# Optimization experiments

Measured on AMD Instinct MI355X. Metric: run time of the kernel, lower is better.

Reference implementation:

```python
import jax, jax.numpy as jnp
import numpy as np

B, N, D = 8, 2048, 128  # D = d + 2
N_LAYER, N_HEAD = 4, 8
PARAMS_STD = 0.05


def _attention(V, Q, Z):
    # V, Q: [D, D]; Z: [B, N, D]
    n = Z.shape[1]
    Attn = jnp.einsum('bni,ij,bmj->bnm', Z, Q, Z)      # [B, N, N]
    values = jnp.einsum('ij,bnj->bni', V, Z)            # [B, N, D]
    return jnp.einsum('bnm,bmi->bni', Attn, values) / n


def setup_inputs() -> dict:
    key = jax.random.key(0)
    kz, kv, kq = jax.random.split(key, 3)
    Z = jax.random.normal(kz, (B, N, D), dtype=jnp.float32)
    v_matrix = PARAMS_STD * jax.random.normal(kv, (N_LAYER, N_HEAD, 1, D, D), dtype=jnp.float32)
    q_matrix = PARAMS_STD * jax.random.normal(kq, (N_LAYER, N_HEAD, 1, D, D), dtype=jnp.float32)
    return {"Z": Z, "v_matrix": v_matrix, "q_matrix": q_matrix}


def reference(Z, v_matrix, q_matrix):
    n_layer, n_head = v_matrix.shape[0], v_matrix.shape[1]
    for i in range(n_layer):
        Zi = Z
        residues = jnp.zeros_like(Zi)
        for j in range(n_head):  # fixed small head loop keeps peak memory at one [B,N,N] buffer
            Vij = v_matrix[i, j, 0]
            Qij = q_matrix[i, j, 0]
            residues = residues + _attention(Vij, Qij, Zi)
        Z = Zi + residues / n_head
    return Z
```

## Files before the change

kernel.cpp:

```cpp
#include <hip/hip_runtime.h>


constexpr int B  = 8;
constexpr int N  = 2048;
constexpr int D  = 128;
constexpr int NL = 4;
constexpr int NH = 8;
constexpr int SP = 32;
constexpr int RPS = N / SP;
constexpr int PAD = 132;

__global__ __launch_bounds__(1024, 1) void k_gram(const float* __restrict__ Zl,
                                                  float* __restrict__ Gpart) {
  const int s = blockIdx.x, b = blockIdx.y;
  const int t = threadIdx.x;
  __shared__ float zs[RPS][PAD];
  const float* Zb = Zl + ((size_t)b * N + (size_t)s * RPS) * D;
#pragma unroll
  for (int j = 0; j < 2; ++j) {
    int fi = t + j * 1024;
    int row = fi >> 5, c4 = fi & 31;
    *(float4*)&zs[row][c4 * 4] = ((const float4*)Zb)[fi];
  }
  __syncthreads();
  const int ti = t >> 5, tj = t & 31;
  float g[4][4];
#pragma unroll
  for (int i = 0; i < 4; ++i)
#pragma unroll
    for (int j = 0; j < 4; ++j) g[i][j] = 0.0f;
#pragma unroll 4
  for (int k = 0; k < RPS; ++k) {
    float a[4], bb[4];
    *(float4*)&a[0]  = *(const float4*)&zs[k][ti * 4];
    *(float4*)&bb[0] = *(const float4*)&zs[k][tj * 4];
#pragma unroll
    for (int i = 0; i < 4; ++i)
#pragma unroll
      for (int j = 0; j < 4; ++j)
        g[i][j] = fmaf(a[i], bb[j], g[i][j]);
  }
  float* out = Gpart + ((size_t)b * SP + s) * D * D;
#pragma unroll
  for (int i = 0; i < 4; ++i)
    *(float4*)&out[(ti * 4 + i) * D + tj * 4] =
        make_float4(g[i][0], g[i][1], g[i][2], g[i][3]);
}

__global__ __launch_bounds__(1024, 1) void k_gred(const float* __restrict__ Gpart,
                                                  float* __restrict__ G) {
  const int s = blockIdx.x, b = blockIdx.y;
  const int t = threadIdx.x;
  const int wlin = b * SP + s;
  __shared__ float4 cbuf[8][128];
  const int sq = t >> 7;
  const int f  = t & 127;
  int f4 = wlin * 128 + f;
  int b2 = f4 >> 12, rest = f4 & 4095;
  const float4* src = (const float4*)Gpart;
  float4 a = make_float4(0.f, 0.f, 0.f, 0.f);
#pragma unroll
  for (int k = 0; k < 4; ++k) {
    int sp = sq * 4 + k;
    float4 v = src[(size_t)(b2 * SP + sp) * (D * D / 4) + rest];
    a.x += v.x; a.y += v.y; a.z += v.z; a.w += v.w;
  }
  cbuf[sq][f] = a;
  __syncthreads();
  if (t < 128) {
    float4 acc = make_float4(0.f, 0.f, 0.f, 0.f);
#pragma unroll
    for (int g2 = 0; g2 < 8; ++g2) {
      float4 v = cbuf[g2][t];
      acc.x += v.x; acc.y += v.y; acc.z += v.z; acc.w += v.w;
    }
    ((float4*)G)[wlin * 128 + t] = acc;
  }
}

__global__ __launch_bounds__(1024, 1) void k_qgwv(const float* __restrict__ Ql,
                                                  const float* __restrict__ Vl,
                                                  const float* __restrict__ G,
                                                  float* __restrict__ W) {
  const int s = blockIdx.x, b = blockIdx.y;
  const int t = threadIdx.x;
  __shared__ float cbuf[32][D];
  const float* Gb = G + (size_t)b * D * D;
  const int p0 = s * 4;
  {
    const int h  = t >> 7;
    const int pp = (t >> 6) & 1;
    const int c2 = t & 63;
    const int pa = pp * 2, pb = pp * 2 + 1;
    const float* Qa = Ql + ((size_t)h * D + (p0 + pa)) * D;
    const float* Qb = Ql + ((size_t)h * D + (p0 + pb)) * D;
    float ua0 = 0.f, ua1 = 0.f, ub0 = 0.f, ub1 = 0.f;
    for (int q4 = 0; q4 < 32; ++q4) {
      float4 qa = *(const float4*)&Qa[q4 * 4];
      float4 qb = *(const float4*)&Qb[q4 * 4];
      float2 g0 = *(const float2*)&Gb[(size_t)(q4 * 4 + 0) * D + 2 * c2];
      float2 g1 = *(const float2*)&Gb[(size_t)(q4 * 4 + 1) * D + 2 * c2];
      float2 g2 = *(const float2*)&Gb[(size_t)(q4 * 4 + 2) * D + 2 * c2];
      float2 g3 = *(const float2*)&Gb[(size_t)(q4 * 4 + 3) * D + 2 * c2];
      ua0 = fmaf(qa.x, g0.x, ua0); ua1 = fmaf(qa.x, g0.y, ua1);
      ub0 = fmaf(qb.x, g0.x, ub0); ub1 = fmaf(qb.x, g0.y, ub1);
      ua0 = fmaf(qa.y, g1.x, ua0); ua1 = fmaf(qa.y, g1.y, ua1);
      ub0 = fmaf(qb.y, g1.x, ub0); ub1 = fmaf(qb.y, g1.y, ub1);
      ua0 = fmaf(qa.z, g2.x, ua0); ua1 = fmaf(qa.z, g2.y, ua1);
      ub0 = fmaf(qb.z, g2.x, ub0); ub1 = fmaf(qb.z, g2.y, ub1);
      ua0 = fmaf(qa.w, g3.x, ua0); ua1 = fmaf(qa.w, g3.y, ua1);
      ub0 = fmaf(qb.w, g3.x, ub0); ub1 = fmaf(qb.w, g3.y, ub1);
    }
    *(float2*)&cbuf[h * 4 + pa][2 * c2] = make_float2(ua0, ua1);
    *(float2*)&cbuf[h * 4 + pb][2 * c2] = make_float2(ub0, ub1);
  }
  __syncthreads();
  {
    const int w = t >> 6, lane = t & 63;
    const float scale = 1.0f / ((float)N * (float)NH);
    float* Wb = W + (size_t)b * D * D;
    for (int ii = 0; ii < 8; ++ii) {
      const int i = w * 8 + ii;
      float a0 = 0.f, a1 = 0.f, a2 = 0.f, a3 = 0.f;
#pragma unroll
      for (int h = 0; h < NH; ++h) {
        float2 v  = *(const float2*)&Vl[((size_t)h * D + i) * D + 2 * lane];
        float2 u0 = *(const float2*)&cbuf[h * 4 + 0][2 * lane];
        float2 u1 = *(const float2*)&cbuf[h * 4 + 1][2 * lane];
        float2 u2 = *(const float2*)&cbuf[h * 4 + 2][2 * lane];
        float2 u3 = *(const float2*)&cbuf[h * 4 + 3][2 * lane];
        a0 = fmaf(u0.x, v.x, a0); a0 = fmaf(u0.y, v.y, a0);
        a1 = fmaf(u1.x, v.x, a1); a1 = fmaf(u1.y, v.y, a1);
        a2 = fmaf(u2.x, v.x, a2); a2 = fmaf(u2.y, v.y, a2);
        a3 = fmaf(u3.x, v.x, a3); a3 = fmaf(u3.y, v.y, a3);
      }
#pragma unroll
      for (int off = 32; off >= 1; off >>= 1) {
        a0 += __shfl_xor(a0, off, 64);
        a1 += __shfl_xor(a1, off, 64);
        a2 += __shfl_xor(a2, off, 64);
        a3 += __shfl_xor(a3, off, 64);
      }
      if (lane == 0) {
        Wb[(size_t)(p0 + 0) * D + i] = a0 * scale;
        Wb[(size_t)(p0 + 1) * D + i] = a1 * scale;
        Wb[(size_t)(p0 + 2) * D + i] = a2 * scale;
        Wb[(size_t)(p0 + 3) * D + i] = a3 * scale;
      }
    }
  }
}

__global__ __launch_bounds__(1024, 1) void k_upd(const float* __restrict__ W,
                                                 const float* __restrict__ Zl,
                                                 float* __restrict__ Zout) {
  const int s = blockIdx.x, b = blockIdx.y;
  const int t = threadIdx.x;
  __shared__ float zs[RPS][PAD];
  const float* Zb = Zl + ((size_t)b * N + (size_t)s * RPS) * D;
#pragma unroll
  for (int j = 0; j < 2; ++j) {
    int fi = t + j * 1024;
    int row = fi >> 5, c4 = fi & 31;
    *(float4*)&zs[row][c4 * 4] = ((const float4*)Zb)[fi];
  }
  __syncthreads();
  const float* Wb = W + (size_t)b * D * D;
  const int ni = t >> 5, ii = t & 31;
  const int n0 = ni * 2;
  float acc[2][4];
#pragma unroll
  for (int i = 0; i < 2; ++i) {
    float4 z0 = *(const float4*)&zs[n0 + i][ii * 4];
    acc[i][0] = z0.x; acc[i][1] = z0.y; acc[i][2] = z0.z; acc[i][3] = z0.w;
  }
#pragma unroll 2
  for (int p4 = 0; p4 < 32; ++p4) {
    float wreg[4][4];
#pragma unroll
    for (int k = 0; k < 4; ++k)
      *(float4*)wreg[k] = *(const float4*)&Wb[(size_t)(p4 * 4 + k) * D + ii * 4];
#pragma unroll
    for (int i = 0; i < 2; ++i) {
      float zreg[4];
      *(float4*)zreg = *(const float4*)&zs[n0 + i][p4 * 4];
#pragma unroll
      for (int k = 0; k < 4; ++k)
#pragma unroll
        for (int c = 0; c < 4; ++c)
          acc[i][c] = fmaf(zreg[k], wreg[k][c], acc[i][c]);
    }
  }
  float* Zo = Zout + ((size_t)b * N + (size_t)s * RPS) * D;
#pragma unroll
  for (int i = 0; i < 2; ++i)
    *(float4*)&Zo[(size_t)(n0 + i) * D + ii * 4] =
        make_float4(acc[i][0], acc[i][1], acc[i][2], acc[i][3]);
}

extern "C" void kernel_launch(void* const* d_in, const int* in_sizes, int n_in,
                              void* d_out, int out_size, void* d_ws, size_t ws_size,
                              hipStream_t stream) {
  const float* Zin = (const float*)d_in[0];
  const float* Vm  = (const float*)d_in[1];
  const float* Qm  = (const float*)d_in[2];
  float* Zout = (float*)d_out;

  char* ws = (char*)d_ws;
  float* Gpart = (float*)ws;
  float* G     = (float*)(ws + (size_t)B * SP * D * D * sizeof(float));
  float* W     = (float*)(ws + (size_t)B * SP * D * D * sizeof(float)
                             + (size_t)B * D * D * sizeof(float));

  const float* Zl = Zin;
  for (int l = 0; l < NL; ++l) {
    const float* Ql = Qm + (size_t)l * NH * D * D;
    const float* Vl = Vm + (size_t)l * NH * D * D;
    k_gram<<<dim3(SP, B), 1024, 0, stream>>>(Zl, Gpart);
    k_gred<<<dim3(SP, B), 1024, 0, stream>>>(Gpart, G);
    k_qgwv<<<dim3(SP, B), 1024, 0, stream>>>(Ql, Vl, G, W);
    k_upd <<<dim3(SP, B), 1024, 0, stream>>>(W, Zl, Zout);
    Zl = Zout;
  }
}
```

Before: 326.3 us.

## Fuse next layer's Gram partials into update kernel and stage G in LDS

```diff
diff --git a/kernel.cpp b/kernel.cpp
--- a/kernel.cpp
+++ b/kernel.cpp
@@ -10,8 +10,8 @@
 constexpr int RPS = N / SP;
 constexpr int PAD = 132;
 
-__global__ __launch_bounds__(1024, 1) void k_gram(const float* __restrict__ Zl,
-                                                  float* __restrict__ Gpart) {
+__global__ __launch_bounds__(1024, 1) void k_gram0(const float* __restrict__ Zl,
+                                                   float* __restrict__ Gpart) {
   const int s = blockIdx.x, b = blockIdx.y;
   const int t = threadIdx.x;
   __shared__ float zs[RPS][PAD];
@@ -84,6 +84,7 @@
                                                   float* __restrict__ W) {
   const int s = blockIdx.x, b = blockIdx.y;
   const int t = threadIdx.x;
+  __shared__ float gs[32][D];
   __shared__ float cbuf[32][D];
   const float* Gb = G + (size_t)b * D * D;
   const int p0 = s * 4;
@@ -95,21 +96,30 @@
     const float* Qa = Ql + ((size_t)h * D + (p0 + pa)) * D;
     const float* Qb = Ql + ((size_t)h * D + (p0 + pb)) * D;
     float ua0 = 0.f, ua1 = 0.f, ub0 = 0.f, ub1 = 0.f;
-    for (int q4 = 0; q4 < 32; ++q4) {
-      float4 qa = *(const float4*)&Qa[q4 * 4];
-      float4 qb = *(const float4*)&Qb[q4 * 4];
-      float2 g0 = *(const float2*)&Gb[(size_t)(q4 * 4 + 0) * D + 2 * c2];
-      float2 g1 = *(const float2*)&Gb[(size_t)(q4 * 4 + 1) * D + 2 * c2];
-      float2 g2 = *(const float2*)&Gb[(size_t)(q4 * 4 + 2) * D + 2 * c2];
-      float2 g3 = *(const float2*)&Gb[(size_t)(q4 * 4 + 3) * D + 2 * c2];
-      ua0 = fmaf(qa.x, g0.x, ua0); ua1 = fmaf(qa.x, g0.y, ua1);
-      ub0 = fmaf(qb.x, g0.x, ub0); ub1 = fmaf(qb.x, g0.y, ub1);
-      ua0 = fmaf(qa.y, g1.x, ua0); ua1 = fmaf(qa.y, g1.y, ua1);
-      ub0 = fmaf(qb.y, g1.x, ub0); ub1 = fmaf(qb.y, g1.y, ub1);
-      ua0 = fmaf(qa.z, g2.x, ua0); ua1 = fmaf(qa.z, g2.y, ua1);
-      ub0 = fmaf(qb.z, g2.x, ub0); ub1 = fmaf(qb.z, g2.y, ub1);
-      ua0 = fmaf(qa.w, g3.x, ua0); ua1 = fmaf(qa.w, g3.y, ua1);
-      ub0 = fmaf(qb.w, g3.x, ub0); ub1 = fmaf(qb.w, g3.y, ub1);
+    const int srow = t >> 5, sc4 = t & 31;
+    for (int qc = 0; qc < 4; ++qc) {
+      __syncthreads();
+      *(float4*)&gs[srow][sc4 * 4] = ((const float4*)(Gb + (size_t)qc * 32 * D))[t];
+      __syncthreads();
+      const float* Qac = Qa + qc * 32;
+      const float* Qbc = Qb + qc * 32;
+#pragma unroll
+      for (int q4 = 0; q4 < 8; ++q4) {
+        float4 qa = *(const float4*)&Qac[q4 * 4];
+        float4 qb = *(const float4*)&Qbc[q4 * 4];
+        float2 g0 = *(const float2*)&gs[q4 * 4 + 0][2 * c2];
+        float2 g1 = *(const float2*)&gs[q4 * 4 + 1][2 * c2];
+        float2 g2 = *(const float2*)&gs[q4 * 4 + 2][2 * c2];
+        float2 g3 = *(const float2*)&gs[q4 * 4 + 3][2 * c2];
+        ua0 = fmaf(qa.x, g0.x, ua0); ua1 = fmaf(qa.x, g0.y, ua1);
+        ub0 = fmaf(qb.x, g0.x, ub0); ub1 = fmaf(qb.x, g0.y, ub1);
+        ua0 = fmaf(qa.y, g1.x, ua0); ua1 = fmaf(qa.y, g1.y, ua1);
+        ub0 = fmaf(qb.y, g1.x, ub0); ub1 = fmaf(qb.y, g1.y, ub1);
+        ua0 = fmaf(qa.z, g2.x, ua0); ua1 = fmaf(qa.z, g2.y, ua1);
+        ub0 = fmaf(qb.z, g2.x, ub0); ub1 = fmaf(qb.z, g2.y, ub1);
+        ua0 = fmaf(qa.w, g3.x, ua0); ua1 = fmaf(qa.w, g3.y, ua1);
+        ub0 = fmaf(qb.w, g3.x, ub0); ub1 = fmaf(qb.w, g3.y, ub1);
+      }
     }
     *(float2*)&cbuf[h * 4 + pa][2 * c2] = make_float2(ua0, ua1);
     *(float2*)&cbuf[h * 4 + pb][2 * c2] = make_float2(ub0, ub1);
@@ -151,9 +161,11 @@
   }
 }
 
-__global__ __launch_bounds__(1024, 1) void k_upd(const float* __restrict__ W,
-                                                 const float* __restrict__ Zl,
-                                                 float* __restrict__ Zout) {
+__global__ __launch_bounds__(1024, 1) void k_updg(const float* __restrict__ W,
+                                                  const float* __restrict__ Zl,
+                                                  float* __restrict__ Zout,
+                                                  float* __restrict__ Gpart,
+                                                  int compute_g) {
   const int s = blockIdx.x, b = blockIdx.y;
   const int t = threadIdx.x;
   __shared__ float zs[RPS][PAD];
@@ -191,11 +203,38 @@
           acc[i][c] = fmaf(zreg[k], wreg[k][c], acc[i][c]);
     }
   }
+  __syncthreads();
   float* Zo = Zout + ((size_t)b * N + (size_t)s * RPS) * D;
 #pragma unroll
-  for (int i = 0; i < 2; ++i)
-    *(float4*)&Zo[(size_t)(n0 + i) * D + ii * 4] =
-        make_float4(acc[i][0], acc[i][1], acc[i][2], acc[i][3]);
+  for (int i = 0; i < 2; ++i) {
+    float4 v = make_float4(acc[i][0], acc[i][1], acc[i][2], acc[i][3]);
+    *(float4*)&zs[n0 + i][ii * 4] = v;
+    *(float4*)&Zo[(size_t)(n0 + i) * D + ii * 4] = v;
+  }
+  if (!compute_g) return;
+  __syncthreads();
+  const int ti = t >> 5, tj = t & 31;
+  float g[4][4];
+#pragma unroll
+  for (int i = 0; i < 4; ++i)
+#pragma unroll
+    for (int j = 0; j < 4; ++j) g[i][j] = 0.0f;
+#pragma unroll 4
+  for (int k = 0; k < RPS; ++k) {
+    float a[4], bb[4];
+    *(float4*)&a[0]  = *(const float4*)&zs[k][ti * 4];
+    *(float4*)&bb[0] = *(const float4*)&zs[k][tj * 4];
+#pragma unroll
+    for (int i = 0; i < 4; ++i)
+#pragma unroll
+      for (int j = 0; j < 4; ++j)
+        g[i][j] = fmaf(a[i], bb[j], g[i][j]);
+  }
+  float* out = Gpart + ((size_t)b * SP + s) * D * D;
+#pragma unroll
+  for (int i = 0; i < 4; ++i)
+    *(float4*)&out[(ti * 4 + i) * D + tj * 4] =
+        make_float4(g[i][0], g[i][1], g[i][2], g[i][3]);
 }
 
 extern "C" void kernel_launch(void* const* d_in, const int* in_sizes, int n_in,
@@ -212,14 +251,15 @@
   float* W     = (float*)(ws + (size_t)B * SP * D * D * sizeof(float)
                              + (size_t)B * D * D * sizeof(float));
 
+  k_gram0<<<dim3(SP, B), 1024, 0, stream>>>(Zin, Gpart);
+
   const float* Zl = Zin;
   for (int l = 0; l < NL; ++l) {
     const float* Ql = Qm + (size_t)l * NH * D * D;
     const float* Vl = Vm + (size_t)l * NH * D * D;
-    k_gram<<<dim3(SP, B), 1024, 0, stream>>>(Zl, Gpart);
     k_gred<<<dim3(SP, B), 1024, 0, stream>>>(Gpart, G);
     k_qgwv<<<dim3(SP, B), 1024, 0, stream>>>(Ql, Vl, G, W);
-    k_upd <<<dim3(SP, B), 1024, 0, stream>>>(W, Zl, Zout);
+    k_updg<<<dim3(SP, B), 1024, 0, stream>>>(W, Zl, Zout, Gpart, (l < NL - 1) ? 1 : 0);
     Zl = Zout;
   }
 }
```

New measurement: 277.6 us. 1.18x faster.
